# Kernel tuning notes

Hardware: AMD Instinct MI355X
Metric: run time of the kernel (lower is better)

Reference implementation:

```python
import jax, jax.numpy as jnp
import numpy as np

N = 50000


def gcn_conv(x, W, b, src, dst, deg_inv_sqrt):
    # h = x @ W, then symmetric-normalized aggregation with self-loops
    h = x @ W  # [N, out]
    norm = deg_inv_sqrt[src] * deg_inv_sqrt[dst]  # [E]
    agg = jax.ops.segment_sum(h[src] * norm[:, None], dst, num_segments=N)
    # self-loop contribution: norm_ii = deg_inv_sqrt[i]^2
    agg = agg + h * (deg_inv_sqrt * deg_inv_sqrt)[:, None]
    return agg + b


def setup_inputs() -> dict:
    key = jax.random.key(0)
    ks = jax.random.split(key, 8)
    F_in, H, C = 128, 128, 64
    x = jax.random.normal(ks[0], (N, F_in), dtype=jnp.float32)
    edge_index = jax.random.randint(ks[1], (2, 800000), 0, N, dtype=jnp.int64)
    s = 1.0 / np.sqrt(F_in)
    W1 = jax.random.uniform(ks[2], (F_in, H), jnp.float32, -s, s)
    b1 = jnp.zeros((H,), jnp.float32)
    W2 = jax.random.uniform(ks[3], (H, H), jnp.float32, -s, s)
    b2 = jnp.zeros((H,), jnp.float32)
    W3 = jax.random.uniform(ks[4], (H, C), jnp.float32, -s, s)
    b3 = jnp.zeros((C,), jnp.float32)
    return {"x": x, "edge_index": edge_index, "W1": W1, "b1": b1,
            "W2": W2, "b2": b2, "W3": W3, "b3": b3}


def reference(x, edge_index, W1, b1, W2, b2, W3, b3):
    src, dst = edge_index[0], edge_index[1]
    # degree with self-loops (edge weight 1): deg[i] = in-degree + 1
    deg = jnp.zeros((N,), x.dtype).at[dst].add(1.0) + 1.0
    dinv = jax.lax.rsqrt(deg)
    h = gcn_conv(x, W1, b1, src, dst, dinv)
    h = jax.nn.relu(h)  # dropout p=0 / eval -> identity
    h = gcn_conv(h, W2, b2, src, dst, dinv)
    h = jax.nn.relu(h)
    h = gcn_conv(h, W3, b3, src, dst, dinv)
    return jax.nn.log_softmax(h, axis=-1)
```

## Files before the change

kernel.cpp:

```cpp
#include <hip/hip_runtime.h>
#include <math.h>

typedef short short8 __attribute__((ext_vector_type(8)));
typedef float floatx4 __attribute__((ext_vector_type(4)));

__device__ __forceinline__ float4 ld4(const float* p) { return *reinterpret_cast<const float4*>(p); }
__device__ __forceinline__ void st4(float* p, float4 v) { *reinterpret_cast<float4*>(p) = v; }

__device__ __forceinline__ float bf2f(unsigned int u) { return __uint_as_float(u << 16); }
__device__ __forceinline__ unsigned int f2bf1(float f) {
    unsigned int x = __float_as_uint(f);
    return (x + 0x7fffu + ((x >> 16) & 1u)) >> 16;
}
__device__ __forceinline__ unsigned int f2bf2(float lo, float hi) {
    return f2bf1(lo) | (f2bf1(hi) << 16);
}
__device__ __forceinline__ void unpack8(uint4 v, float* f) {
    f[0] = bf2f(v.x & 0xffffu); f[1] = bf2f(v.x >> 16);
    f[2] = bf2f(v.y & 0xffffu); f[3] = bf2f(v.y >> 16);
    f[4] = bf2f(v.z & 0xffffu); f[5] = bf2f(v.z >> 16);
    f[6] = bf2f(v.w & 0xffffu); f[7] = bf2f(v.w >> 16);
}

__global__ __launch_bounds__(256) void k_count_prep(const int* __restrict__ dst, int* __restrict__ deg,
                                                    int* __restrict__ rank, int E, int nbE,
                                                    const float* __restrict__ W1, const float* __restrict__ W2,
                                                    const float* __restrict__ W3, unsigned short* __restrict__ Wt1,
                                                    unsigned short* __restrict__ Wt2, unsigned short* __restrict__ Wt3) {
    if ((int)blockIdx.x < nbE) {
        int e = blockIdx.x * 256 + threadIdx.x;
        if (e < E) rank[e] = atomicAdd(&deg[dst[e]], 1);
    } else {
        int t = (blockIdx.x - nbE) * 256 + threadIdx.x;
        if (t < 16384) {
            int k = t & 127, n = t >> 7;
            Wt1[n * 128 + k] = (unsigned short)f2bf1(W1[(size_t)k * 128 + n]);
        } else if (t < 32768) {
            int u = t - 16384;
            int k = u & 127, n = u >> 7;
            Wt2[n * 128 + k] = (unsigned short)f2bf1(W2[(size_t)k * 128 + n]);
        } else if (t < 40960) {
            int u = t - 32768;
            int k = u & 127, n = u >> 7;
            Wt3[n * 128 + k] = (unsigned short)f2bf1(W3[(size_t)k * 64 + n]);
        }
    }
}

__global__ __launch_bounds__(256) void k_reduce_gemm1(const int* __restrict__ deg, int* __restrict__ bsum, int n, int nb,
                                                      const float* __restrict__ X, const unsigned short* __restrict__ Wt,
                                                      unsigned short* __restrict__ O, int nrows) {
    constexpr int LDR = 136;
    __shared__ __align__(16) unsigned char smem[(64 * LDR + 128 * LDR) * 2];

    const int tid = threadIdx.x;
    if ((int)blockIdx.x < nb) {
        int* s = (int*)smem;
        int i = blockIdx.x * 256 + tid;
        s[tid] = (i < n) ? deg[i] : 0;
        __syncthreads();
        for (int off = 128; off > 0; off >>= 1) {
            if (tid < off) s[tid] += s[tid + off];
            __syncthreads();
        }
        if (tid == 0) bsum[blockIdx.x] = s[0];
        return;
    }

    unsigned short* sX = (unsigned short*)smem;
    unsigned short* sB = sX + 64 * LDR;
    const int row0 = (blockIdx.x - nb) * 64;

#pragma unroll
    for (int i = 0; i < 4; ++i) {
        int idx = tid + i * 256;
        int r = idx >> 4, c8 = idx & 15;
        int grow = row0 + r;
        uint4 v = make_uint4(0, 0, 0, 0);
        if (grow < nrows) {
            float4 a = ld4(X + (size_t)grow * 128 + c8 * 8);
            float4 b = ld4(X + (size_t)grow * 128 + c8 * 8 + 4);
            v = make_uint4(f2bf2(a.x, a.y), f2bf2(a.z, a.w), f2bf2(b.x, b.y), f2bf2(b.z, b.w));
        }
        *reinterpret_cast<uint4*>(&sX[r * LDR + c8 * 8]) = v;
    }
#pragma unroll
    for (int i = 0; i < 8; ++i) {
        int idx = tid + i * 256;
        int nn = idx >> 4, c8 = idx & 15;
        *reinterpret_cast<uint4*>(&sB[nn * LDR + c8 * 8]) =
            *reinterpret_cast<const uint4*>(Wt + (size_t)nn * 128 + c8 * 8);
    }
    __syncthreads();

    const int lane = tid & 63;
    const int wave = tid >> 6;
    const int l15  = lane & 15;
    const int quad = lane >> 4;

    floatx4 acc[8];
#pragma unroll
    for (int j = 0; j < 8; ++j) acc[j] = (floatx4){0.f, 0.f, 0.f, 0.f};

    const unsigned short* xbase = &sX[(wave * 16 + l15) * LDR + quad * 8];
#pragma unroll
    for (int kk = 0; kk < 4; ++kk) {
        short8 xb = *reinterpret_cast<const short8*>(xbase + kk * 32);
#pragma unroll
        for (int j = 0; j < 8; ++j) {
            short8 wa = *reinterpret_cast<const short8*>(&sB[(j * 16 + l15) * LDR + quad * 8 + kk * 32]);
            acc[j] = __builtin_amdgcn_mfma_f32_16x16x32_bf16(wa, xb, acc[j], 0, 0, 0);
        }
    }

    int xrow = row0 + wave * 16 + l15;
    if (xrow < nrows) {
#pragma unroll
        for (int j = 0; j < 8; ++j) {
            uint2 o = make_uint2(f2bf2(acc[j][0], acc[j][1]), f2bf2(acc[j][2], acc[j][3]));
            *reinterpret_cast<uint2*>(O + (size_t)xrow * 128 + j * 16 + quad * 4) = o;
        }
    }
}

__global__ __launch_bounds__(256) void k_scan_small(const int* __restrict__ bsum, int* __restrict__ boff, int nb) {
    __shared__ int s[256];
    int t = threadIdx.x;
    int v = (t < nb) ? bsum[t] : 0;
    s[t] = v;
    __syncthreads();
    for (int off = 1; off < 256; off <<= 1) {
        int x = (t >= off) ? s[t - off] : 0;
        __syncthreads();
        s[t] += x;
        __syncthreads();
    }
    if (t < nb) boff[t] = s[t] - v;
}

__global__ __launch_bounds__(256) void k_scan_final(const int* __restrict__ deg, const int* __restrict__ boff,
                                                    int* __restrict__ row_off, float* __restrict__ dinv, int n) {
    __shared__ int s[256];
    int t = threadIdx.x;
    int i = blockIdx.x * 256 + t;
    int v = (i < n) ? deg[i] : 0;
    s[t] = v;
    __syncthreads();
    for (int off = 1; off < 256; off <<= 1) {
        int x = (t >= off) ? s[t - off] : 0;
        __syncthreads();
        s[t] += x;
        __syncthreads();
    }
    int incl = s[t] + boff[blockIdx.x];
    if (i < n) {
        row_off[i] = incl - v;
        dinv[i]    = 1.0f / sqrtf((float)v + 1.0f);
        if (i == n - 1) row_off[n] = incl;
    }
}

__global__ __launch_bounds__(256) void k_fill(const int* __restrict__ src, const int* __restrict__ dst,
                                              const int* __restrict__ rank, const int* __restrict__ roff,
                                              const float* __restrict__ dinv, int2* __restrict__ cpair, int E) {
    int e = blockIdx.x * 256 + threadIdx.x;
    if (e < E) {
        int s = src[e], d = dst[e];
        int pos = roff[d] + rank[e];
        cpair[pos] = make_int2(s, __float_as_int(dinv[s] * dinv[d]));
    }
}

template <int NC>
__global__ __launch_bounds__(256) void k_gemm_mfma(const unsigned short* __restrict__ X,
                                                   const unsigned short* __restrict__ Wt,
                                                   unsigned short* __restrict__ O, int nrows) {
    constexpr int LDR = 136;
    __shared__ unsigned short sX[64 * LDR];
    __shared__ unsigned short sB[NC * LDR];

    const int tid  = threadIdx.x;
    const int row0 = blockIdx.x * 64;

#pragma unroll
    for (int i = 0; i < 4; ++i) {
        int idx = tid + i * 256;
        int r = idx >> 4, c8 = idx & 15;
        int grow = row0 + r;
        uint4 v = make_uint4(0, 0, 0, 0);
        if (grow < nrows) v = *reinterpret_cast<const uint4*>(X + (size_t)grow * 128 + c8 * 8);
        *reinterpret_cast<uint4*>(&sX[r * LDR + c8 * 8]) = v;
    }
#pragma unroll
    for (int i = 0; i < NC / 16; ++i) {
        int idx = tid + i * 256;
        int n = idx >> 4, c8 = idx & 15;
        *reinterpret_cast<uint4*>(&sB[n * LDR + c8 * 8]) =
            *reinterpret_cast<const uint4*>(Wt + (size_t)n * 128 + c8 * 8);
    }
    __syncthreads();

    const int lane = tid & 63;
    const int wave = tid >> 6;
    const int l15  = lane & 15;
    const int quad = lane >> 4;

    floatx4 acc[NC / 16];
#pragma unroll
    for (int j = 0; j < NC / 16; ++j) acc[j] = (floatx4){0.f, 0.f, 0.f, 0.f};

    const unsigned short* xbase = &sX[(wave * 16 + l15) * LDR + quad * 8];
#pragma unroll
    for (int kk = 0; kk < 4; ++kk) {
        short8 xb = *reinterpret_cast<const short8*>(xbase + kk * 32);
#pragma unroll
        for (int j = 0; j < NC / 16; ++j) {
            short8 wa = *reinterpret_cast<const short8*>(&sB[(j * 16 + l15) * LDR + quad * 8 + kk * 32]);
            acc[j] = __builtin_amdgcn_mfma_f32_16x16x32_bf16(wa, xb, acc[j], 0, 0, 0);
        }
    }

    int xrow = row0 + wave * 16 + l15;
    if (xrow < nrows) {
#pragma unroll
        for (int j = 0; j < NC / 16; ++j) {
            uint2 o = make_uint2(f2bf2(acc[j][0], acc[j][1]), f2bf2(acc[j][2], acc[j][3]));
            *reinterpret_cast<uint2*>(O + (size_t)xrow * NC + j * 16 + quad * 4) = o;
        }
    }
}

__global__ __launch_bounds__(256) void k_agg_relu(const unsigned short* __restrict__ H, const int* __restrict__ roff,
                                                  const int2* __restrict__ cpair, const float* __restrict__ dinv,
                                                  const float* __restrict__ bias, unsigned short* __restrict__ O, int n) {
    int t    = blockIdx.x * 256 + threadIdx.x;
    int node = t >> 4;
    int f8   = (t & 15) * 8;
    if (node >= n) return;

    float di = dinv[node];
    float sc = di * di;
    float a[8];
    {
        uint4 hv = *reinterpret_cast<const uint4*>(H + (size_t)node * 128 + f8);
        float h[8];
        unpack8(hv, h);
#pragma unroll
        for (int i = 0; i < 8; ++i) a[i] = h[i] * sc;
    }

    int e  = roff[node];
    int e1 = roff[node + 1];
    for (; e + 3 < e1; e += 4) {
        int2 p[4];
        uint4 v[4];
#pragma unroll
        for (int u = 0; u < 4; ++u) p[u] = cpair[e + u];
#pragma unroll
        for (int u = 0; u < 4; ++u) v[u] = *reinterpret_cast<const uint4*>(H + (size_t)p[u].x * 128 + f8);
#pragma unroll
        for (int u = 0; u < 4; ++u) {
            float nu = __int_as_float(p[u].y);
            float g[8];
            unpack8(v[u], g);
#pragma unroll
            for (int i = 0; i < 8; ++i) a[i] += g[i] * nu;
        }
    }
    for (; e < e1; ++e) {
        int2 p0 = cpair[e];
        float n0 = __int_as_float(p0.y);
        uint4 v0 = *reinterpret_cast<const uint4*>(H + (size_t)p0.x * 128 + f8);
        float g0[8];
        unpack8(v0, g0);
#pragma unroll
        for (int i = 0; i < 8; ++i) a[i] += g0[i] * n0;
    }

    float4 b0 = ld4(bias + f8);
    float4 b1 = ld4(bias + f8 + 4);
    float bb[8] = {b0.x, b0.y, b0.z, b0.w, b1.x, b1.y, b1.z, b1.w};
#pragma unroll
    for (int i = 0; i < 8; ++i) a[i] = fmaxf(a[i] + bb[i], 0.0f);

    uint4 ov = make_uint4(f2bf2(a[0], a[1]), f2bf2(a[2], a[3]), f2bf2(a[4], a[5]), f2bf2(a[6], a[7]));
    *reinterpret_cast<uint4*>(O + (size_t)node * 128 + f8) = ov;
}

__global__ __launch_bounds__(256) void k_agg_softmax(const unsigned short* __restrict__ H, const int* __restrict__ roff,
                                                     const int2* __restrict__ cpair, const float* __restrict__ dinv,
                                                     const float* __restrict__ bias, float* __restrict__ O, int n) {
    int t    = blockIdx.x * 256 + threadIdx.x;
    int node = t >> 3;
    int f8   = (t & 7) * 8;
    if (node >= n) return;

    float di = dinv[node];
    float sc = di * di;
    float a[8];
    {
        uint4 hv = *reinterpret_cast<const uint4*>(H + (size_t)node * 64 + f8);
        float h[8];
        unpack8(hv, h);
#pragma unroll
        for (int i = 0; i < 8; ++i) a[i] = h[i] * sc;
    }

    int e  = roff[node];
    int e1 = roff[node + 1];
    for (; e + 7 < e1; e += 8) {
        int2 pr[8];
        uint4 v[8];
#pragma unroll
        for (int u = 0; u < 8; ++u) pr[u] = cpair[e + u];
#pragma unroll
        for (int u = 0; u < 8; ++u) v[u] = *reinterpret_cast<const uint4*>(H + (size_t)pr[u].x * 64 + f8);
#pragma unroll
        for (int u = 0; u < 8; ++u) {
            float nu = __int_as_float(pr[u].y);
            float gg[8];
            unpack8(v[u], gg);
#pragma unroll
            for (int i = 0; i < 8; ++i) a[i] += gg[i] * nu;
        }
    }
    if (e + 3 < e1) {
        int2 pr[4];
        uint4 v[4];
#pragma unroll
        for (int u = 0; u < 4; ++u) pr[u] = cpair[e + u];
#pragma unroll
        for (int u = 0; u < 4; ++u) v[u] = *reinterpret_cast<const uint4*>(H + (size_t)pr[u].x * 64 + f8);
#pragma unroll
        for (int u = 0; u < 4; ++u) {
            float nu = __int_as_float(pr[u].y);
            float gg[8];
            unpack8(v[u], gg);
#pragma unroll
            for (int i = 0; i < 8; ++i) a[i] += gg[i] * nu;
        }
        e += 4;
    }
    for (; e < e1; ++e) {
        int2 p0 = cpair[e];
        float n0 = __int_as_float(p0.y);
        uint4 v0 = *reinterpret_cast<const uint4*>(H + (size_t)p0.x * 64 + f8);
        float g0[8];
        unpack8(v0, g0);
#pragma unroll
        for (int i = 0; i < 8; ++i) a[i] += g0[i] * n0;
    }

    float4 b0 = ld4(bias + f8);
    float4 b1 = ld4(bias + f8 + 4);
    float bb[8] = {b0.x, b0.y, b0.z, b0.w, b1.x, b1.y, b1.z, b1.w};
    float v[8];
#pragma unroll
    for (int i = 0; i < 8; ++i) v[i] = a[i] + bb[i];

    float m = v[0];
#pragma unroll
    for (int i = 1; i < 8; ++i) m = fmaxf(m, v[i]);
    m = fmaxf(m, __shfl_xor(m, 1));
    m = fmaxf(m, __shfl_xor(m, 2));
    m = fmaxf(m, __shfl_xor(m, 4));

    float ssum = 0.0f;
#pragma unroll
    for (int i = 0; i < 8; ++i) ssum += expf(v[i] - m);
    ssum += __shfl_xor(ssum, 1);
    ssum += __shfl_xor(ssum, 2);
    ssum += __shfl_xor(ssum, 4);
    float ls = logf(ssum);

    float* op = O + (size_t)node * 64 + f8;
    st4(op, make_float4(v[0] - m - ls, v[1] - m - ls, v[2] - m - ls, v[3] - m - ls));
    st4(op + 4, make_float4(v[4] - m - ls, v[5] - m - ls, v[6] - m - ls, v[7] - m - ls));
}

extern "C" void kernel_launch(void* const* d_in, const int* in_sizes, int n_in,
                              void* d_out, int out_size, void* d_ws, size_t ws_size,
                              hipStream_t stream) {
    const float* x  = (const float*)d_in[0];
    const int*   ei = (const int*)d_in[1];
    const float* W1 = (const float*)d_in[2];
    const float* b1 = (const float*)d_in[3];
    const float* W2 = (const float*)d_in[4];
    const float* b2 = (const float*)d_in[5];
    const float* W3 = (const float*)d_in[6];
    const float* b3 = (const float*)d_in[7];
    float* out = (float*)d_out;

    const int N = in_sizes[0] / 128;
    const int E = in_sizes[1] / 2;
    const int* src = ei;
    const int* dst = ei + E;

    char* ws = (char*)d_ws;
    size_t off = 0;
    auto alloc = [&](size_t bytes) -> char* {
        char* p = ws + off;
        off = (off + bytes + 255) & ~(size_t)255;
        return p;
    };
    int nb  = (N + 255) / 256;
    int nbE = (E + 255) / 256;
    int blocks64 = (N + 63) / 64;

    int*   deg     = (int*)alloc((size_t)N * 4);
    int*   row_off = (int*)alloc(((size_t)N + 1) * 4);
    float* dinv    = (float*)alloc((size_t)N * 4);
    int*   bsum    = (int*)alloc((size_t)nb * 4);
    int*   boff    = (int*)alloc((size_t)nb * 4);
    int*   rank    = (int*)alloc((size_t)E * 4);
    int2*  cpair   = (int2*)alloc((size_t)E * 8);
    unsigned short* Wt1  = (unsigned short*)alloc(128 * 128 * 2);
    unsigned short* Wt2  = (unsigned short*)alloc(128 * 128 * 2);
    unsigned short* Wt3  = (unsigned short*)alloc(64 * 128 * 2);
    unsigned short* bufA = (unsigned short*)alloc((size_t)N * 128 * 2);
    unsigned short* bufB = (unsigned short*)alloc((size_t)N * 128 * 2);
    unsigned short* bufC = (unsigned short*)alloc((size_t)N * 64 * 2);
    (void)ws_size; (void)n_in; (void)out_size;

    hipMemsetAsync(deg, 0, (size_t)N * 4, stream);
    k_count_prep<<<nbE + 160, 256, 0, stream>>>(dst, deg, rank, E, nbE, W1, W2, W3, Wt1, Wt2, Wt3);
    k_reduce_gemm1<<<nb + blocks64, 256, 0, stream>>>(deg, bsum, N, nb, x, Wt1, bufA, N);
    k_scan_small<<<1, 256, 0, stream>>>(bsum, boff, nb);
    k_scan_final<<<nb, 256, 0, stream>>>(deg, boff, row_off, dinv, N);
    k_fill<<<nbE, 256, 0, stream>>>(src, dst, rank, row_off, dinv, cpair, E);

    k_agg_relu<<<((size_t)N * 16 + 255) / 256, 256, 0, stream>>>(bufA, row_off, cpair, dinv, b1, bufB, N);
    k_gemm_mfma<128><<<blocks64, 256, 0, stream>>>(bufB, Wt2, bufA, N);
    k_agg_relu<<<((size_t)N * 16 + 255) / 256, 256, 0, stream>>>(bufA, row_off, cpair, dinv, b2, bufB, N);
    k_gemm_mfma<64><<<blocks64, 256, 0, stream>>>(bufB, Wt3, bufC, N);
    k_agg_softmax<<<((size_t)N * 8 + 255) / 256, 256, 0, stream>>>(bufC, row_off, cpair, dinv, b3, out, N);
}
```

Baseline: 256.3 us.

## Factor symmetric normalization into pre-scaled features and drop per-edge weights

Rewrites the normalization D^-1/2 A D^-1/2 as a row pre-scale of H by dinv (folded into the GEMM epilogues, plus a separate scaling pass for the first layer's output) and a post-scale of the aggregate by dinv[node]. The CSR then stores only source indices (4 bytes per edge instead of 8), which halves edge-list traffic in each aggregation and removes a multiply per edge. The cost is an extra read-modify-write pass over bufA merged into the fill kernel, and one more bf16 rounding of the pre-scaled features, which adds a little numerical error.

Measured after the change: 252.3 us. About the same (-1.6%).

```diff
diff --git a/kernel.cpp b/kernel.cpp
--- a/kernel.cpp
+++ b/kernel.cpp
@@ -160,20 +160,33 @@
     }
 }
 
-__global__ __launch_bounds__(256) void k_fill(const int* __restrict__ src, const int* __restrict__ dst,
-                                              const int* __restrict__ rank, const int* __restrict__ roff,
-                                              const float* __restrict__ dinv, int2* __restrict__ cpair, int E) {
-    int e = blockIdx.x * 256 + threadIdx.x;
-    if (e < E) {
-        int s = src[e], d = dst[e];
-        int pos = roff[d] + rank[e];
-        cpair[pos] = make_int2(s, __float_as_int(dinv[s] * dinv[d]));
+__global__ __launch_bounds__(256) void k_fill_scale(const int* __restrict__ src, const int* __restrict__ dst,
+                                                    const int* __restrict__ rank, const int* __restrict__ roff,
+                                                    int* __restrict__ csrc, int E, int nbE,
+                                                    unsigned short* __restrict__ A, const float* __restrict__ dinv,
+                                                    int n16) {
+    if ((int)blockIdx.x < nbE) {
+        int e = blockIdx.x * 256 + threadIdx.x;
+        if (e < E) csrc[roff[dst[e]] + rank[e]] = src[e];
+    } else {
+        int idx = (blockIdx.x - nbE) * 256 + threadIdx.x;
+        if (idx < n16) {
+            float di = dinv[idx >> 4];
+            uint4 v = *reinterpret_cast<const uint4*>(A + (size_t)idx * 8);
+            float f[8];
+            unpack8(v, f);
+#pragma unroll
+            for (int i = 0; i < 8; ++i) f[i] *= di;
+            uint4 o = make_uint4(f2bf2(f[0], f[1]), f2bf2(f[2], f[3]), f2bf2(f[4], f[5]), f2bf2(f[6], f[7]));
+            *reinterpret_cast<uint4*>(A + (size_t)idx * 8) = o;
+        }
     }
 }
 
 template <int NC>
 __global__ __launch_bounds__(256) void k_gemm_mfma(const unsigned short* __restrict__ X,
                                                    const unsigned short* __restrict__ Wt,
+                                                   const float* __restrict__ dinv,
                                                    unsigned short* __restrict__ O, int nrows) {
     constexpr int LDR = 136;
     __shared__ unsigned short sX[64 * LDR];
@@ -222,141 +235,127 @@
 
     int xrow = row0 + wave * 16 + l15;
     if (xrow < nrows) {
+        float di = dinv[xrow];
 #pragma unroll
         for (int j = 0; j < NC / 16; ++j) {
-            uint2 o = make_uint2(f2bf2(acc[j][0], acc[j][1]), f2bf2(acc[j][2], acc[j][3]));
+            uint2 o = make_uint2(f2bf2(acc[j][0] * di, acc[j][1] * di), f2bf2(acc[j][2] * di, acc[j][3] * di));
             *reinterpret_cast<uint2*>(O + (size_t)xrow * NC + j * 16 + quad * 4) = o;
         }
     }
 }
 
 __global__ __launch_bounds__(256) void k_agg_relu(const unsigned short* __restrict__ H, const int* __restrict__ roff,
-                                                  const int2* __restrict__ cpair, const float* __restrict__ dinv,
+                                                  const int* __restrict__ csrc, const float* __restrict__ dinv,
                                                   const float* __restrict__ bias, unsigned short* __restrict__ O, int n) {
     int t    = blockIdx.x * 256 + threadIdx.x;
     int node = t >> 4;
     int f8   = (t & 15) * 8;
     if (node >= n) return;
 
-    float di = dinv[node];
-    float sc = di * di;
     float a[8];
     {
         uint4 hv = *reinterpret_cast<const uint4*>(H + (size_t)node * 128 + f8);
-        float h[8];
-        unpack8(hv, h);
-#pragma unroll
-        for (int i = 0; i < 8; ++i) a[i] = h[i] * sc;
+        unpack8(hv, a);
     }
 
     int e  = roff[node];
     int e1 = roff[node + 1];
     for (; e + 3 < e1; e += 4) {
-        int2 p[4];
+        int s[4];
         uint4 v[4];
 #pragma unroll
-        for (int u = 0; u < 4; ++u) p[u] = cpair[e + u];
-#pragma unroll
-        for (int u = 0; u < 4; ++u) v[u] = *reinterpret_cast<const uint4*>(H + (size_t)p[u].x * 128 + f8);
+        for (int u = 0; u < 4; ++u) s[u] = csrc[e + u];
+#pragma unroll
+        for (int u = 0; u < 4; ++u) v[u] = *reinterpret_cast<const uint4*>(H + (size_t)s[u] * 128 + f8);
 #pragma unroll
         for (int u = 0; u < 4; ++u) {
-            float nu = __int_as_float(p[u].y);
             float g[8];
             unpack8(v[u], g);
 #pragma unroll
-            for (int i = 0; i < 8; ++i) a[i] += g[i] * nu;
+            for (int i = 0; i < 8; ++i) a[i] += g[i];
         }
     }
     for (; e < e1; ++e) {
-        int2 p0 = cpair[e];
-        float n0 = __int_as_float(p0.y);
-        uint4 v0 = *reinterpret_cast<const uint4*>(H + (size_t)p0.x * 128 + f8);
+        uint4 v0 = *reinterpret_cast<const uint4*>(H + (size_t)csrc[e] * 128 + f8);
         float g0[8];
         unpack8(v0, g0);
 #pragma unroll
-        for (int i = 0; i < 8; ++i) a[i] += g0[i] * n0;
-    }
-
+        for (int i = 0; i < 8; ++i) a[i] += g0[i];
+    }
+
+    float di = dinv[node];
     float4 b0 = ld4(bias + f8);
     float4 b1 = ld4(bias + f8 + 4);
     float bb[8] = {b0.x, b0.y, b0.z, b0.w, b1.x, b1.y, b1.z, b1.w};
 #pragma unroll
-    for (int i = 0; i < 8; ++i) a[i] = fmaxf(a[i] + bb[i], 0.0f);
+    for (int i = 0; i < 8; ++i) a[i] = fmaxf(a[i] * di + bb[i], 0.0f);
 
     uint4 ov = make_uint4(f2bf2(a[0], a[1]), f2bf2(a[2], a[3]), f2bf2(a[4], a[5]), f2bf2(a[6], a[7]));
     *reinterpret_cast<uint4*>(O + (size_t)node * 128 + f8) = ov;
 }
 
 __global__ __launch_bounds__(256) void k_agg_softmax(const unsigned short* __restrict__ H, const int* __restrict__ roff,
-                                                     const int2* __restrict__ cpair, const float* __restrict__ dinv,
+                                                     const int* __restrict__ csrc, const float* __restrict__ dinv,
                                                      const float* __restrict__ bias, float* __restrict__ O, int n) {
     int t    = blockIdx.x * 256 + threadIdx.x;
     int node = t >> 3;
     int f8   = (t & 7) * 8;
     if (node >= n) return;
 
-    float di = dinv[node];
-    float sc = di * di;
     float a[8];
     {
         uint4 hv = *reinterpret_cast<const uint4*>(H + (size_t)node * 64 + f8);
-        float h[8];
-        unpack8(hv, h);
-#pragma unroll
-        for (int i = 0; i < 8; ++i) a[i] = h[i] * sc;
+        unpack8(hv, a);
     }
 
     int e  = roff[node];
     int e1 = roff[node + 1];
     for (; e + 7 < e1; e += 8) {
-        int2 pr[8];
+        int s[8];
         uint4 v[8];
 #pragma unroll
-        for (int u = 0; u < 8; ++u) pr[u] = cpair[e + u];
-#pragma unroll
-        for (int u = 0; u < 8; ++u) v[u] = *reinterpret_cast<const uint4*>(H + (size_t)pr[u].x * 64 + f8);
+        for (int u = 0; u < 8; ++u) s[u] = csrc[e + u];
+#pragma unroll
+        for (int u = 0; u < 8; ++u) v[u] = *reinterpret_cast<const uint4*>(H + (size_t)s[u] * 64 + f8);
 #pragma unroll
         for (int u = 0; u < 8; ++u) {
-            float nu = __int_as_float(pr[u].y);
             float gg[8];
             unpack8(v[u], gg);
 #pragma unroll
-            for (int i = 0; i < 8; ++i) a[i] += gg[i] * nu;
+            for (int i = 0; i < 8; ++i) a[i] += gg[i];
         }
     }
     if (e + 3 < e1) {
-        int2 pr[4];
+        int s[4];
         uint4 v[4];
 #pragma unroll
-        for (int u = 0; u < 4; ++u) pr[u] = cpair[e + u];
-#pragma unroll
-        for (int u = 0; u < 4; ++u) v[u] = *reinterpret_cast<const uint4*>(H + (size_t)pr[u].x * 64 + f8);
+        for (int u = 0; u < 4; ++u) s[u] = csrc[e + u];
+#pragma unroll
+        for (int u = 0; u < 4; ++u) v[u] = *reinterpret_cast<const uint4*>(H + (size_t)s[u] * 64 + f8);
 #pragma unroll
         for (int u = 0; u < 4; ++u) {
-            float nu = __int_as_float(pr[u].y);
             float gg[8];
             unpack8(v[u], gg);
 #pragma unroll
-            for (int i = 0; i < 8; ++i) a[i] += gg[i] * nu;
+            for (int i = 0; i < 8; ++i) a[i] += gg[i];
         }
         e += 4;
     }
     for (; e < e1; ++e) {
-        int2 p0 = cpair[e];
-        float n0 = __int_as_float(p0.y);
-        uint4 v0 = *reinterpret_cast<const uint4*>(H + (size_t)p0.x * 64 + f8);
+        uint4 v0 = *reinterpret_cast<const uint4*>(H + (size_t)csrc[e] * 64 + f8);
         float g0[8];
         unpack8(v0, g0);
 #pragma unroll
-        for (int i = 0; i < 8; ++i) a[i] += g0[i] * n0;
-    }
-
+        for (int i = 0; i < 8; ++i) a[i] += g0[i];
+    }
+
+    float di = dinv[node];
     float4 b0 = ld4(bias + f8);
     float4 b1 = ld4(bias + f8 + 4);
     float bb[8] = {b0.x, b0.y, b0.z, b0.w, b1.x, b1.y, b1.z, b1.w};
     float v[8];
 #pragma unroll
-    for (int i = 0; i < 8; ++i) v[i] = a[i] + bb[i];
+    for (int i = 0; i < 8; ++i) v[i] = a[i] * di + bb[i];
 
     float m = v[0];
 #pragma unroll
@@ -406,6 +405,8 @@
     int nb  = (N + 255) / 256;
     int nbE = (E + 255) / 256;
     int blocks64 = (N + 63) / 64;
+    int n16 = N * 16;
+    int nbS = (n16 + 255) / 256;
 
     int*   deg     = (int*)alloc((size_t)N * 4);
     int*   row_off = (int*)alloc(((size_t)N + 1) * 4);
@@ -413,7 +414,7 @@
     int*   bsum    = (int*)alloc((size_t)nb * 4);
     int*   boff    = (int*)alloc((size_t)nb * 4);
     int*   rank    = (int*)alloc((size_t)E * 4);
-    int2*  cpair   = (int2*)alloc((size_t)E * 8);
+    int*   csrc    = (int*)alloc((size_t)E * 4);
     unsigned short* Wt1  = (unsigned short*)alloc(128 * 128 * 2);
     unsigned short* Wt2  = (unsigned short*)alloc(128 * 128 * 2);
     unsigned short* Wt3  = (unsigned short*)alloc(64 * 128 * 2);
@@ -427,11 +428,11 @@
     k_reduce_gemm1<<<nb + blocks64, 256, 0, stream>>>(deg, bsum, N, nb, x, Wt1, bufA, N);
     k_scan_small<<<1, 256, 0, stream>>>(bsum, boff, nb);
     k_scan_final<<<nb, 256, 0, stream>>>(deg, boff, row_off, dinv, N);
-    k_fill<<<nbE, 256, 0, stream>>>(src, dst, rank, row_off, dinv, cpair, E);
-
-    k_agg_relu<<<((size_t)N * 16 + 255) / 256, 256, 0, stream>>>(bufA, row_off, cpair, dinv, b1, bufB, N);
-    k_gemm_mfma<128><<<blocks64, 256, 0, stream>>>(bufB, Wt2, bufA, N);
-    k_agg_relu<<<((size_t)N * 16 + 255) / 256, 256, 0, stream>>>(bufA, row_off, cpair, dinv, b2, bufB, N);
-    k_gemm_mfma<64><<<blocks64, 256, 0, stream>>>(bufB, Wt3, bufC, N);
-    k_agg_softmax<<<((size_t)N * 8 + 255) / 256, 256, 0, stream>>>(bufC, row_off, cpair, dinv, b3, out, N);
-}
+    k_fill_scale<<<nbE + nbS, 256, 0, stream>>>(src, dst, rank, row_off, csrc, E, nbE, bufA, dinv, n16);
+
+    k_agg_relu<<<((size_t)N * 16 + 255) / 256, 256, 0, stream>>>(bufA, row_off, csrc, dinv, b1, bufB, N);
+    k_gemm_mfma<128><<<blocks64, 256, 0, stream>>>(bufB, Wt2, dinv, bufA, N);
+    k_agg_relu<<<((size_t)N * 16 + 255) / 256, 256, 0, stream>>>(bufA, row_off, csrc, dinv, b2, bufB, N);
+    k_gemm_mfma<64><<<blocks64, 256, 0, stream>>>(bufB, Wt3, dinv, bufC, N);
+    k_agg_softmax<<<((size_t)N * 8 + 255) / 256, 256, 0, stream>>>(bufC, row_off, csrc, dinv, b3, out, N);
+}
```
